# Kernel tuning notes

Hardware: AMD Instinct MI355X
Metric: run time of the kernel (lower is better)

Reference implementation:

```python
import jax, jax.numpy as jnp
import numpy as np

HEADS = 8
D_MODEL = 512
T_LEN = 12
WINDOW = 3
N_NODES = 325
BATCH = 4
HDIM = D_MODEL // HEADS
LN_EPS = 1e-5


def _shift_list(T, W):
    # matches get_shift_list: circular left shifts by W, W-1, ..., 1
    idxs = np.arange(T)
    return np.stack([(idxs + i) % T for i in range(-W, 0)])  # [W, T]


def setup_inputs() -> dict:
    key = jax.random.key(0)
    ks = jax.random.split(key, 13)
    s = 1.0 / np.sqrt(D_MODEL)
    return {
        "x": jax.random.normal(ks[0], (BATCH, T_LEN, N_NODES, D_MODEL), jnp.float32),
        "adj": jax.random.uniform(ks[1], (BATCH, T_LEN, N_NODES, N_NODES), jnp.float32),
        "s_adj": jax.random.normal(ks[2], (BATCH, N_NODES, N_NODES), jnp.float32),
        "Wq": jax.random.normal(ks[3], (D_MODEL, D_MODEL), jnp.float32) * s,
        "bq": jax.random.normal(ks[4], (D_MODEL,), jnp.float32) * 0.01,
        "Wk": jax.random.normal(ks[5], (D_MODEL, D_MODEL), jnp.float32) * s,
        "bk": jax.random.normal(ks[6], (D_MODEL,), jnp.float32) * 0.01,
        "Wv": jax.random.normal(ks[7], (D_MODEL, D_MODEL), jnp.float32) * s,
        "bv": jax.random.normal(ks[8], (D_MODEL,), jnp.float32) * 0.01,
        "Wd": jax.random.normal(ks[9], (T_LEN, T_LEN * WINDOW), jnp.float32) * (1.0 / np.sqrt(T_LEN * WINDOW)),
        "bd": jax.random.normal(ks[10], (T_LEN,), jnp.float32) * 0.01,
        "gamma": jnp.ones((D_MODEL,), jnp.float32),
        "beta": jnp.zeros((D_MODEL,), jnp.float32),
    }


def reference(x, adj, s_adj, Wq, bq, Wk, bk, Wv, bv, Wd, bd, gamma, beta):
    B, T, N, D = x.shape
    H, hd = HEADS, D // HEADS
    shifts = _shift_list(T, WINDOW)  # static numpy indices

    def proj(W_, b_):
        y = jnp.einsum("btnd,ed->btne", x, W_) + b_  # Linear: x @ W.T + b
        return y.reshape(B, T, N, H, hd).transpose(0, 1, 3, 2, 4)  # [B,T,H,N,hd]

    q = proj(Wq, bq)
    k = proj(Wk, bk)
    v = proj(Wv, bv)

    # Faithful to the original: q scaling and k/v shifts ACCUMULATE across
    # window iterations (q,k,v are reassigned in the torch loop); adj is
    # re-indexed from the original tensor each iteration.
    scale = 1.0 / jnp.asarray(np.sqrt(hd), x.dtype)
    hs = []
    qc, kc, vc = q, k, v
    for ti in range(WINDOW):
        qc = qc * scale
        s_idx = shifts[ti]
        kc = kc[:, s_idx]
        vc = vc[:, s_idx]
        a = jnp.einsum("bthnd,bthmd->bthnm", qc, kc)  # [B,T,H,N,N]
        a = (a + 1.0) * adj[:, s_idx][:, :, None, :, :]  # broadcast over heads
        a = jax.nn.softmax(a, axis=-1)
        r = jnp.einsum("bthnm,bthmd->bthnd", a, vc)
        hs.append(r.transpose(0, 1, 3, 2, 4).reshape(B, T, N, D))

    h = jnp.concatenate(hs, axis=1)          # [B, W*T, N, D]
    h = h.transpose(0, 2, 3, 1)              # [B, N, D, W*T]
    h = jnp.einsum("bndw,tw->bndt", h, Wd) + bd  # dense over time axis
    h = h.transpose(0, 3, 1, 2)              # [B, T, N, D]
    # dropout is identity at inference
    y = h + x
    mu = jnp.mean(y, axis=-1, keepdims=True)
    var = jnp.mean((y - mu) ** 2, axis=-1, keepdims=True)
    return (y - mu) / jnp.sqrt(var + LN_EPS) * gamma + beta
```

## Files before the change

### kernel.cpp

```cpp
#include <hip/hip_runtime.h>
#include <stdint.h>

#define HEADS 8
#define DM 512
#define TT 12
#define WIN 3
#define NN 325
#define BB 4
#define HD 64
#define MROWS (BB*TT*NN)
#define NSLAB (BB*TT*HEADS)
#define NKT 11
static const size_t QKV_ELE = (size_t)MROWS * DM;
static const size_t FRAG_SLAB = (size_t)NKT * 4 * 64 * 8;

typedef unsigned short u16;
typedef __attribute__((ext_vector_type(8))) short bf16x8;
typedef __attribute__((ext_vector_type(4))) float f32x4;

#define MFMA(a,b,c) __builtin_amdgcn_mfma_f32_16x16x32_bf16(a, b, c, 0, 0, 0)
#define LG2E 1.44269504f
#define C8F  (-11.5415603f)

static __device__ __forceinline__ float ex2(float x) {
  float r; asm("v_exp_f32 %0, %1" : "=v"(r) : "v"(x)); return r;
}

static __device__ __forceinline__ u16 f2bf(float f) {
  uint32_t u = __float_as_uint(f);
  u += 0x7fff + ((u >> 16) & 1);
  return (u16)(u >> 16);
}
static __device__ __forceinline__ uint32_t pk2(float hi, float lo) {
  return __builtin_amdgcn_perm(__float_as_uint(hi), __float_as_uint(lo), 0x07060302);
}
static __device__ __forceinline__ float bf2f(u16 h) {
  return __uint_as_float((uint32_t)h << 16);
}

typedef const __attribute__((address_space(1))) unsigned int* gas1;
typedef __attribute__((address_space(3))) unsigned int* las3;
static __device__ __forceinline__ void gll16(const void* g, void* l) {
  __builtin_amdgcn_global_load_lds((gas1)g, (las3)l, 16, 0, 0);
}

__global__ void pack_w(const float* __restrict__ Wq, const float* __restrict__ Wk,
                       const float* __restrict__ Wv, const float* __restrict__ bq,
                       const float* __restrict__ bk, const float* __restrict__ bv,
                       u16* __restrict__ Wb, float* __restrict__ biasc) {
  int i = blockIdx.x * blockDim.x + threadIdx.x;
  const int n4 = (3 * 512 * 512) / 4;
  if (i < n4) {
    int j = i << 2;
    int which = j >> 18;
    int off4 = i & ((512 * 512 / 4) - 1);
    const float* src = which == 0 ? Wq : (which == 1 ? Wk : Wv);
    float4 v = ((const float4*)src)[off4];
    uint32_t a0 = (uint32_t)f2bf(v.x) | ((uint32_t)f2bf(v.y) << 16);
    uint32_t a1 = (uint32_t)f2bf(v.z) | ((uint32_t)f2bf(v.w) << 16);
    ((uint2*)Wb)[i] = make_uint2(a0, a1);
  }
  if (i < 1536 / 4) {
    int j = i << 2;
    int which = j >> 9;
    int off4 = i & 127;
    const float* src = which == 0 ? bq : (which == 1 ? bk : bv);
    ((float4*)biasc)[i] = ((const float4*)src)[off4];
  }
}

__global__ __launch_bounds__(256) void proj_gemm(
    const float* __restrict__ x,
    const u16* __restrict__ W,
    const float* __restrict__ bias,
    u16* __restrict__ qkv)
{
  __shared__ u16 sA[128 * 32];
  __shared__ u16 sB[128 * 32];
  const int m0 = blockIdx.x * 128;
  const int n0 = blockIdx.y * 128;
  const int tid = threadIdx.x;
  const int lane = tid & 63;
  const int wid = tid >> 6;
  const int wr = wid >> 1, wc = wid & 1;

  f32x4 acc[4][4] = {};

  const int srow = tid >> 2;
  const int scol = (tid & 3) * 8;

  for (int k0 = 0; k0 < 512; k0 += 32) {
    __syncthreads();
#pragma unroll
    for (int i = 0; i < 2; ++i) {
      int row = i * 64 + srow;
      int gm = m0 + row; if (gm >= MROWS) gm = MROWS - 1;
      const float* xa = x + (size_t)gm * 512 + k0 + scol;
      float4 f0 = *(const float4*)xa;
      float4 f1 = *(const float4*)(xa + 4);
      uint4 u;
      u.x = pk2(f0.y, f0.x);
      u.y = pk2(f0.w, f0.z);
      u.z = pk2(f1.y, f1.x);
      u.w = pk2(f1.w, f1.z);
      *(uint4*)&sA[row * 32 + scol] = u;
      *(bf16x8*)&sB[row * 32 + scol] = *(const bf16x8*)&W[(size_t)(n0 + row) * 512 + k0 + scol];
    }
    __syncthreads();
    bf16x8 af[4], bfr[4];
#pragma unroll
    for (int mi = 0; mi < 4; ++mi)
      af[mi] = *(const bf16x8*)&sA[(wr * 64 + mi * 16 + (lane & 15)) * 32 + (lane >> 4) * 8];
#pragma unroll
    for (int ni = 0; ni < 4; ++ni)
      bfr[ni] = *(const bf16x8*)&sB[(wc * 64 + ni * 16 + (lane & 15)) * 32 + (lane >> 4) * 8];
#pragma unroll
    for (int mi = 0; mi < 4; ++mi)
#pragma unroll
      for (int ni = 0; ni < 4; ++ni)
        acc[mi][ni] = MFMA(af[mi], bfr[ni], acc[mi][ni]);
  }

  const int lr = (lane >> 4) * 4;
  const int lc = lane & 15;
#pragma unroll
  for (int mi = 0; mi < 4; ++mi) {
#pragma unroll
    for (int j = 0; j < 4; ++j) {
      int gm = m0 + wr * 64 + mi * 16 + lr + j;
      if (gm < MROWS) {
        int b = gm / (TT * NN);
        int rem = gm - b * (TT * NN);
        int t = rem / NN;
        int n = rem - t * NN;
#pragma unroll
        for (int ni = 0; ni < 4; ++ni) {
          int e = n0 + wc * 64 + ni * 16 + lc;
          float val = acc[mi][ni][j] + bias[e];
          int which = e >> 9;
          int h = (e >> 6) & 7;
          int d = e & 63;
          qkv[(size_t)which * QKV_ELE + ((((size_t)(b * TT + t) * HEADS + h) * NN + n) << 6) + d] = f2bf(val);
        }
      }
    }
  }
}

__global__ __launch_bounds__(256) void kv_pack(const u16* __restrict__ qkv,
                                               u16* __restrict__ kf, u16* __restrict__ vf) {
  int slab = blockIdx.x;
  const u16* K = qkv + QKV_ELE + ((size_t)slab * NN << 6);
  const u16* V = qkv + 2 * QKV_ELE + ((size_t)slab * NN << 6);
  u16* kout = kf + (size_t)slab * FRAG_SLAB;
  u16* vout = vf + (size_t)slab * FRAG_SLAB;
  int t = threadIdx.x;
  int f = t >> 6;
  int lane = t & 63;
  int qi = lane & 15, g = lane >> 4;
  int krow_l = ((qi >> 2) << 3) + (qi & 3) + ((f >> 1) << 2);
  int kd = ((f & 1) << 5) + g * 8;
  for (int kt = 0; kt < NKT; ++kt) {
    int row = kt * 32 + krow_l;
    bf16x8 kv = {};
    if (row < NN) kv = *(const bf16x8*)(K + ((size_t)row << 6) + kd);
    *(bf16x8*)(kout + ((size_t)kt * 4 + f) * 512 + lane * 8) = kv;
    union { u16 e[8]; bf16x8 v; } vv;
#pragma unroll
    for (int e = 0; e < 8; ++e) {
      int vrow = kt * 32 + g * 8 + e;
      vv.e[e] = (vrow < NN) ? V[((size_t)vrow << 6) + f * 16 + qi] : (u16)0;
    }
    *(bf16x8*)(vout + ((size_t)kt * 4 + f) * 512 + lane * 8) = vv.v;
  }
}

__global__ __launch_bounds__(256) void adj_pack(const float* __restrict__ adj,
                                                float* __restrict__ adjp) {
  int blk = blockIdx.x;
  int kt = blk % 11;
  int rest = blk / 11;
  int qt = rest % 6;
  int slab = rest / 6;
  const float* src = adj + (size_t)slab * NN * NN;
  float* dst = adjp + (size_t)blk * 2048;
  int t = threadIdx.x;
  int s = t >> 6, lane = t & 63;
  int qi = lane & 15, g = lane >> 4;
  int row = qt * 64 + s * 16 + qi; if (row > NN - 1) row = NN - 1;
  int c0 = kt * 32 + g * 8;
  const float* sp = src + (size_t)row * NN;
  float v[8];
#pragma unroll
  for (int e = 0; e < 8; ++e) {
    int c = c0 + e;
    v[e] = (c < NN) ? __builtin_fmaf(sp[c], LG2E, C8F) : C8F;
  }
  float4 w0 = {v[0], v[1], v[2], v[3]};
  float4 w1 = {v[4], v[5], v[6], v[7]};
  *(float4*)(dst + t * 8) = w0;
  *(float4*)(dst + t * 8 + 4) = w1;
}

__global__ __launch_bounds__(256, 2) void attn(
    const u16* __restrict__ q,
    const u16* __restrict__ kf,
    const u16* __restrict__ vf,
    const float* __restrict__ adjp,
    u16* __restrict__ hcat)
{
  __shared__ u16 kvlds[4][2][2][4][512];

  const int tid = threadIdx.x;
  const int wid = tid >> 6;
  const int lane = tid & 63;
  const int qi = lane & 15;
  const int g = lane >> 4;

  int ord = (blockIdx.x & 7) * 216 + (blockIdx.x >> 3);
  int slab = ord / 36;
  int inner = ord - slab * 36;
  int b = slab / 12;
  int ta = slab - b * 12;
  int ti = inner / 12;
  int r2 = inner - ti * 12;
  int qt = r2 >> 1;
  int hg = r2 & 1;

  int tadd = ti == 0 ? 3 : (ti == 1 ? 2 : 1);
  int ckv  = ti == 0 ? 9 : (ti == 1 ? 7 : 6);
  float qsc = ti == 0 ? 0.125f : (ti == 1 ? 0.015625f : 0.001953125f);
  int t = ta + tadd; if (t >= 12) t -= 12;
  int t_kv = t + ckv; if (t_kv >= 12) t_kv -= 12;
  int h = hg * 4 + wid;
  int q0 = qt * 64;

  const float nqC8 = -qsc * C8F;

  const u16* qbase = q + ((((size_t)(b * TT + t) * HEADS + h) * NN) << 6);
  int kvslab = (b * TT + t_kv) * HEADS + h;
  const u16* kfb = kf + (size_t)kvslab * FRAG_SLAB + lane * 8;
  const u16* vfb = vf + (size_t)kvslab * FRAG_SLAB + lane * 8;
  const float* apb = adjp + (size_t)(slab * 6 + qt) * (11 * 2048) + lane * 8;

  bf16x8 qf[4][2];
#pragma unroll
  for (int s = 0; s < 4; ++s) {
    int qr = q0 + s * 16 + qi; if (qr > NN - 1) qr = NN - 1;
    const u16* qp = qbase + ((size_t)qr << 6) + g * 8;
    qf[s][0] = *(const bf16x8*)qp;
    qf[s][1] = *(const bf16x8*)(qp + 32);
  }

  const f32x4 z4 = {0.f, 0.f, 0.f, 0.f};

  f32x4 acc[4][4] = {};
  float lsum[4] = {0.f, 0.f, 0.f, 0.f};

#pragma unroll
  for (int f = 0; f < 4; ++f) {
    gll16(kfb + (size_t)f * 512, &kvlds[wid][0][0][f][0]);
    gll16(vfb + (size_t)f * 512, &kvlds[wid][0][1][f][0]);
  }
  float4 fa[4], fb4[4];
#pragma unroll
  for (int s = 0; s < 4; ++s) {
    fa[s]  = *(const float4*)(apb + s * 512);
    fb4[s] = *(const float4*)(apb + s * 512 + 4);
  }

  for (int kt = 0; kt < 11; ++kt) {
    int cur = kt & 1;
    float4 fan[4], fbn[4];
    if (kt < 10) {
      const u16* kp = kfb + (size_t)(kt + 1) * 2048;
      const u16* vp = vfb + (size_t)(kt + 1) * 2048;
#pragma unroll
      for (int f = 0; f < 4; ++f) {
        gll16(kp + (size_t)f * 512, &kvlds[wid][cur ^ 1][0][f][0]);
        gll16(vp + (size_t)f * 512, &kvlds[wid][cur ^ 1][1][f][0]);
      }
      const float* ap = apb + (size_t)(kt + 1) * 2048;
#pragma unroll
      for (int s = 0; s < 4; ++s) {
        fan[s] = *(const float4*)(ap + s * 512);
        fbn[s] = *(const float4*)(ap + s * 512 + 4);
      }
      asm volatile("s_waitcnt vmcnt(16)" ::: "memory");
    } else {
      asm volatile("s_waitcnt vmcnt(0)" ::: "memory");
    }

    bf16x8 kc[4], vc[4];
#pragma unroll
    for (int f = 0; f < 4; ++f) {
      kc[f] = *(const bf16x8*)&kvlds[wid][cur][0][f][lane * 8];
      vc[f] = *(const bf16x8*)&kvlds[wid][cur][1][f][lane * 8];
    }

#pragma unroll
    for (int s = 0; s < 4; ++s) {
      f32x4 s0 = MFMA(kc[0], qf[s][0], z4);
      s0 = MFMA(kc[1], qf[s][1], s0);
      f32x4 s1 = MFMA(kc[2], qf[s][0], z4);
      s1 = MFMA(kc[3], qf[s][1], s1);
      float p[8];
      float u, qu;
      u = fa[s].x;  qu = __builtin_fmaf(qsc, u, nqC8); p[0] = ex2(__builtin_fmaf(s0[0], qu, u));
      u = fa[s].y;  qu = __builtin_fmaf(qsc, u, nqC8); p[1] = ex2(__builtin_fmaf(s0[1], qu, u));
      u = fa[s].z;  qu = __builtin_fmaf(qsc, u, nqC8); p[2] = ex2(__builtin_fmaf(s0[2], qu, u));
      u = fa[s].w;  qu = __builtin_fmaf(qsc, u, nqC8); p[3] = ex2(__builtin_fmaf(s0[3], qu, u));
      u = fb4[s].x; qu = __builtin_fmaf(qsc, u, nqC8); p[4] = ex2(__builtin_fmaf(s1[0], qu, u));
      u = fb4[s].y; qu = __builtin_fmaf(qsc, u, nqC8); p[5] = ex2(__builtin_fmaf(s1[1], qu, u));
      u = fb4[s].z; qu = __builtin_fmaf(qsc, u, nqC8); p[6] = ex2(__builtin_fmaf(s1[2], qu, u));
      u = fb4[s].w; qu = __builtin_fmaf(qsc, u, nqC8); p[7] = ex2(__builtin_fmaf(s1[3], qu, u));
      lsum[s] += ((p[0] + p[1]) + (p[2] + p[3])) + ((p[4] + p[5]) + (p[6] + p[7]));
      union { uint32_t u[4]; bf16x8 v; } pu;
      pu.u[0] = pk2(p[1], p[0]);
      pu.u[1] = pk2(p[3], p[2]);
      pu.u[2] = pk2(p[5], p[4]);
      pu.u[3] = pk2(p[7], p[6]);
      acc[s][0] = MFMA(pu.v, vc[0], acc[s][0]);
      acc[s][1] = MFMA(pu.v, vc[1], acc[s][1]);
      acc[s][2] = MFMA(pu.v, vc[2], acc[s][2]);
      acc[s][3] = MFMA(pu.v, vc[3], acc[s][3]);
    }
#pragma unroll
    for (int s = 0; s < 4; ++s) { fa[s] = fan[s]; fb4[s] = fbn[s]; }
  }

  const float padcorr = 27.0f * ex2(C8F);
  size_t hb = ((size_t)(b * 36 + ti * TT + t) * NN) << 9;
#pragma unroll
  for (int s = 0; s < 4; ++s) {
    float v = lsum[s];
    v += __shfl_xor(v, 16);
    v += __shfl_xor(v, 32);
    v -= padcorr;
    float linv = 1.0f / v;
#pragma unroll
    for (int j = 0; j < 4; ++j) {
      float li = __shfl(linv, g * 4 + j);
      int qrow = q0 + s * 16 + 4 * g + j;
      if (qrow < NN) {
        u16* op = hcat + hb + ((size_t)qrow << 9) + h * 64 + qi;
#pragma unroll
        for (int dt = 0; dt < 4; ++dt)
          op[dt * 16] = f2bf(acc[s][dt][j] * li);
      }
    }
  }
}

__global__ __launch_bounds__(256, 4) void mix_ln(
    const u16* __restrict__ hcat,
    const float* __restrict__ Wd,
    const float* __restrict__ bd,
    const float* __restrict__ x,
    const float* __restrict__ gamma,
    const float* __restrict__ beta,
    float* __restrict__ out)
{
  __shared__ u16 sH[36 * 512];
  __shared__ float sWd[12 * 36];
  __shared__ float sred[8];
  int bn = blockIdx.x;
  int b = bn / NN, n = bn - b * NN;
  int tid = threadIdx.x;
  int lane = tid & 63, wid = tid >> 6;

  for (int i = tid; i < 12 * 36; i += 256) sWd[i] = Wd[i];
  for (int i = tid; i < 36 * 128; i += 256) {
    int w = i >> 7, d4 = i & 127;
    *(uint2*)&sH[(w << 9) + (d4 << 2)] =
        *(const uint2*)&hcat[(((size_t)(b * 36 + w) * NN + n) << 9) + (d4 << 2)];
  }
  __syncthreads();

  for (int t = 0; t < TT; ++t) {
    float a0 = 0.f, a1 = 0.f;
#pragma unroll
    for (int w = 0; w < 36; ++w) {
      float wv = sWd[t * 36 + w];
      a0 += bf2f(sH[(w << 9) + tid]) * wv;
      a1 += bf2f(sH[(w << 9) + 256 + tid]) * wv;
    }
    size_t xoff = ((size_t)(b * TT + t) * NN + n) << 9;
    float bdt = bd[t];
    float y0 = a0 + bdt + x[xoff + tid];
    float y1 = a1 + bdt + x[xoff + 256 + tid];
    float s = y0 + y1, ss = y0 * y0 + y1 * y1;
#pragma unroll
    for (int off = 32; off > 0; off >>= 1) {
      s += __shfl_down(s, off);
      ss += __shfl_down(ss, off);
    }
    if (lane == 0) { sred[wid * 2] = s; sred[wid * 2 + 1] = ss; }
    __syncthreads();
    float stot = sred[0] + sred[2] + sred[4] + sred[6];
    float sstot = sred[1] + sred[3] + sred[5] + sred[7];
    float mu = stot * (1.0f / 512.0f);
    float var = sstot * (1.0f / 512.0f) - mu * mu;
    float rstd = rsqrtf(var + 1e-5f);
    out[xoff + tid] = (y0 - mu) * rstd * gamma[tid] + beta[tid];
    out[xoff + 256 + tid] = (y1 - mu) * rstd * gamma[tid + 256] + beta[tid + 256];
    __syncthreads();
  }
}

extern "C" void kernel_launch(void* const* d_in, const int* in_sizes, int n_in,
                              void* d_out, int out_size, void* d_ws, size_t ws_size,
                              hipStream_t stream) {
  const float* x     = (const float*)d_in[0];
  const float* adj   = (const float*)d_in[1];
  const float* Wq    = (const float*)d_in[3];
  const float* bq    = (const float*)d_in[4];
  const float* Wk    = (const float*)d_in[5];
  const float* bk    = (const float*)d_in[6];
  const float* Wv    = (const float*)d_in[7];
  const float* bv    = (const float*)d_in[8];
  const float* Wd    = (const float*)d_in[9];
  const float* bd    = (const float*)d_in[10];
  const float* gamma = (const float*)d_in[11];
  const float* beta  = (const float*)d_in[12];
  float* out = (float*)d_out;

  char* ws = (char*)d_ws;
  size_t off = 0;
  auto alloc = [&](size_t bytes) {
    void* p = ws + off;
    off += (bytes + 255) & ~(size_t)255;
    return p;
  };
  u16* Wb     = (u16*)alloc(1536 * 512 * 2);
  float* bias = (float*)alloc(1536 * 4);
  u16* qkv    = (u16*)alloc(3 * QKV_ELE * 2);
  u16* hcat   = (u16*)alloc(3 * QKV_ELE * 2);
  u16* kfb    = (u16*)alloc((size_t)NSLAB * FRAG_SLAB * 2);
  u16* vfb    = (u16*)alloc((size_t)NSLAB * FRAG_SLAB * 2);
  float* adjp = (float*)alloc((size_t)48 * 6 * 11 * 2048 * 4);

  adj_pack<<<dim3(48 * 6 * 11), dim3(256), 0, stream>>>(adj, adjp);
  pack_w<<<dim3(768), dim3(256), 0, stream>>>(Wq, Wk, Wv, bq, bk, bv, Wb, bias);
  proj_gemm<<<dim3((MROWS + 127) / 128, 1536 / 128), dim3(256), 0, stream>>>(x, Wb, bias, qkv);
  kv_pack<<<dim3(NSLAB), dim3(256), 0, stream>>>(qkv, kfb, vfb);
  attn<<<dim3(BB * TT * WIN * 6 * 2), dim3(256), 0, stream>>>(qkv, kfb, vfb, adjp, hcat);
  mix_ln<<<dim3(BB * NN), dim3(256), 0, stream>>>(hcat, Wd, bd, x, gamma, beta, out);
}
```

Measured before the change: 223.4 us.

## Merge prep kernels, swizzle projection GEMM blocks, make layer-norm wave-per-timestep

Folds the adjacency packing and weight packing into one launch to save a kernel launch. The projection GEMM now uses a 1D grid with an XCD-aware swizzle of block order, which should improve L2 reuse of the weight and activation tiles. mix_ln is restructured so each wave handles whole timesteps with 8 contiguous features per lane: it uses vectorized bf16x8 LDS reads and float4 global loads and stores, and the reduction becomes a wave-level xor shuffle. This removes the per-timestep block barriers and shared-memory reductions. The cost is more registers per thread in mix_ln.

```diff
diff --git a/kernel.cpp b/kernel.cpp
--- a/kernel.cpp
+++ b/kernel.cpp
@@ -44,28 +44,56 @@
   __builtin_amdgcn_global_load_lds((gas1)g, (las3)l, 16, 0, 0);
 }
 
-__global__ void pack_w(const float* __restrict__ Wq, const float* __restrict__ Wk,
-                       const float* __restrict__ Wv, const float* __restrict__ bq,
-                       const float* __restrict__ bk, const float* __restrict__ bv,
-                       u16* __restrict__ Wb, float* __restrict__ biasc) {
-  int i = blockIdx.x * blockDim.x + threadIdx.x;
-  const int n4 = (3 * 512 * 512) / 4;
-  if (i < n4) {
-    int j = i << 2;
-    int which = j >> 18;
-    int off4 = i & ((512 * 512 / 4) - 1);
-    const float* src = which == 0 ? Wq : (which == 1 ? Wk : Wv);
-    float4 v = ((const float4*)src)[off4];
-    uint32_t a0 = (uint32_t)f2bf(v.x) | ((uint32_t)f2bf(v.y) << 16);
-    uint32_t a1 = (uint32_t)f2bf(v.z) | ((uint32_t)f2bf(v.w) << 16);
-    ((uint2*)Wb)[i] = make_uint2(a0, a1);
-  }
-  if (i < 1536 / 4) {
-    int j = i << 2;
-    int which = j >> 9;
-    int off4 = i & 127;
-    const float* src = which == 0 ? bq : (which == 1 ? bk : bv);
-    ((float4*)biasc)[i] = ((const float4*)src)[off4];
+__global__ __launch_bounds__(256) void prep(
+    const float* __restrict__ adj, const float* __restrict__ Wq,
+    const float* __restrict__ Wk, const float* __restrict__ Wv,
+    const float* __restrict__ bq, const float* __restrict__ bk,
+    const float* __restrict__ bv, float* __restrict__ adjp,
+    u16* __restrict__ Wb, float* __restrict__ biasc) {
+  if (blockIdx.x < 3168) {
+    int blk = blockIdx.x;
+    int kt = blk % 11;
+    int rest = blk / 11;
+    int qt = rest % 6;
+    int slab = rest / 6;
+    const float* src = adj + (size_t)slab * NN * NN;
+    float* dst = adjp + (size_t)blk * 2048;
+    int t = threadIdx.x;
+    int s = t >> 6, lane = t & 63;
+    int qi = lane & 15, g = lane >> 4;
+    int row = qt * 64 + s * 16 + qi; if (row > NN - 1) row = NN - 1;
+    int c0 = kt * 32 + g * 8;
+    const float* sp = src + (size_t)row * NN;
+    float v[8];
+#pragma unroll
+    for (int e = 0; e < 8; ++e) {
+      int c = c0 + e;
+      v[e] = (c < NN) ? __builtin_fmaf(sp[c], LG2E, C8F) : C8F;
+    }
+    float4 w0 = {v[0], v[1], v[2], v[3]};
+    float4 w1 = {v[4], v[5], v[6], v[7]};
+    *(float4*)(dst + t * 8) = w0;
+    *(float4*)(dst + t * 8 + 4) = w1;
+  } else {
+    int i = (blockIdx.x - 3168) * 256 + threadIdx.x;
+    const int n4 = (3 * 512 * 512) / 4;
+    if (i < n4) {
+      int j = i << 2;
+      int which = j >> 18;
+      int off4 = i & ((512 * 512 / 4) - 1);
+      const float* src = which == 0 ? Wq : (which == 1 ? Wk : Wv);
+      float4 v = ((const float4*)src)[off4];
+      uint32_t a0 = (uint32_t)f2bf(v.x) | ((uint32_t)f2bf(v.y) << 16);
+      uint32_t a1 = (uint32_t)f2bf(v.z) | ((uint32_t)f2bf(v.w) << 16);
+      ((uint2*)Wb)[i] = make_uint2(a0, a1);
+    }
+    if (i < 1536 / 4) {
+      int j = i << 2;
+      int which = j >> 9;
+      int off4 = i & 127;
+      const float* src = which == 0 ? bq : (which == 1 ? bk : bv);
+      ((float4*)biasc)[i] = ((const float4*)src)[off4];
+    }
   }
 }
 
@@ -77,8 +105,10 @@
 {
   __shared__ u16 sA[128 * 32];
   __shared__ u16 sB[128 * 32];
-  const int m0 = blockIdx.x * 128;
-  const int n0 = blockIdx.y * 128;
+  int bid = blockIdx.x;
+  int ord = (bid & 7) * 183 + (bid >> 3);
+  const int m0 = (ord / 12) * 128;
+  const int n0 = (ord % 12) * 128;
   const int tid = threadIdx.x;
   const int lane = tid & 63;
   const int wid = tid >> 6;
@@ -173,33 +203,6 @@
     }
     *(bf16x8*)(vout + ((size_t)kt * 4 + f) * 512 + lane * 8) = vv.v;
   }
-}
-
-__global__ __launch_bounds__(256) void adj_pack(const float* __restrict__ adj,
-                                                float* __restrict__ adjp) {
-  int blk = blockIdx.x;
-  int kt = blk % 11;
-  int rest = blk / 11;
-  int qt = rest % 6;
-  int slab = rest / 6;
-  const float* src = adj + (size_t)slab * NN * NN;
-  float* dst = adjp + (size_t)blk * 2048;
-  int t = threadIdx.x;
-  int s = t >> 6, lane = t & 63;
-  int qi = lane & 15, g = lane >> 4;
-  int row = qt * 64 + s * 16 + qi; if (row > NN - 1) row = NN - 1;
-  int c0 = kt * 32 + g * 8;
-  const float* sp = src + (size_t)row * NN;
-  float v[8];
-#pragma unroll
-  for (int e = 0; e < 8; ++e) {
-    int c = c0 + e;
-    v[e] = (c < NN) ? __builtin_fmaf(sp[c], LG2E, C8F) : C8F;
-  }
-  float4 w0 = {v[0], v[1], v[2], v[3]};
-  float4 w1 = {v[4], v[5], v[6], v[7]};
-  *(float4*)(dst + t * 8) = w0;
-  *(float4*)(dst + t * 8 + 4) = w1;
 }
 
 __global__ __launch_bounds__(256, 2) void attn(
@@ -363,7 +366,6 @@
 {
   __shared__ u16 sH[36 * 512];
   __shared__ float sWd[12 * 36];
-  __shared__ float sred[8];
   int bn = blockIdx.x;
   int b = bn / NN, n = bn - b * NN;
   int tid = threadIdx.x;
@@ -377,34 +379,53 @@
   }
   __syncthreads();
 
-  for (int t = 0; t < TT; ++t) {
-    float a0 = 0.f, a1 = 0.f;
-#pragma unroll
+  const int d0 = lane * 8;
+  float4 g0 = *(const float4*)&gamma[d0];
+  float4 g1 = *(const float4*)&gamma[d0 + 4];
+  float4 be0 = *(const float4*)&beta[d0];
+  float4 be1 = *(const float4*)&beta[d0 + 4];
+
+  for (int t = wid; t < TT; t += 4) {
+    float a[8] = {};
+    const float* wrow = &sWd[t * 36];
+#pragma unroll 4
     for (int w = 0; w < 36; ++w) {
-      float wv = sWd[t * 36 + w];
-      a0 += bf2f(sH[(w << 9) + tid]) * wv;
-      a1 += bf2f(sH[(w << 9) + 256 + tid]) * wv;
+      float wv = wrow[w];
+      bf16x8 hv = *(const bf16x8*)&sH[(w << 9) + d0];
+#pragma unroll
+      for (int j = 0; j < 8; ++j) a[j] = __builtin_fmaf(bf2f((u16)hv[j]), wv, a[j]);
     }
     size_t xoff = ((size_t)(b * TT + t) * NN + n) << 9;
+    float4 x0 = *(const float4*)&x[xoff + d0];
+    float4 x1 = *(const float4*)&x[xoff + d0 + 4];
     float bdt = bd[t];
-    float y0 = a0 + bdt + x[xoff + tid];
-    float y1 = a1 + bdt + x[xoff + 256 + tid];
-    float s = y0 + y1, ss = y0 * y0 + y1 * y1;
+    float y[8];
+    y[0] = a[0] + bdt + x0.x;  y[1] = a[1] + bdt + x0.y;
+    y[2] = a[2] + bdt + x0.z;  y[3] = a[3] + bdt + x0.w;
+    y[4] = a[4] + bdt + x1.x;  y[5] = a[5] + bdt + x1.y;
+    y[6] = a[6] + bdt + x1.z;  y[7] = a[7] + bdt + x1.w;
+    float s = 0.f, ss = 0.f;
+#pragma unroll
+    for (int j = 0; j < 8; ++j) { s += y[j]; ss = __builtin_fmaf(y[j], y[j], ss); }
 #pragma unroll
     for (int off = 32; off > 0; off >>= 1) {
-      s += __shfl_down(s, off);
-      ss += __shfl_down(ss, off);
-    }
-    if (lane == 0) { sred[wid * 2] = s; sred[wid * 2 + 1] = ss; }
-    __syncthreads();
-    float stot = sred[0] + sred[2] + sred[4] + sred[6];
-    float sstot = sred[1] + sred[3] + sred[5] + sred[7];
-    float mu = stot * (1.0f / 512.0f);
-    float var = sstot * (1.0f / 512.0f) - mu * mu;
+      s += __shfl_xor(s, off);
+      ss += __shfl_xor(ss, off);
+    }
+    float mu = s * (1.0f / 512.0f);
+    float var = ss * (1.0f / 512.0f) - mu * mu;
     float rstd = rsqrtf(var + 1e-5f);
-    out[xoff + tid] = (y0 - mu) * rstd * gamma[tid] + beta[tid];
-    out[xoff + 256 + tid] = (y1 - mu) * rstd * gamma[tid + 256] + beta[tid + 256];
-    __syncthreads();
+    float4 o0, o1;
+    o0.x = (y[0] - mu) * rstd * g0.x + be0.x;
+    o0.y = (y[1] - mu) * rstd * g0.y + be0.y;
+    o0.z = (y[2] - mu) * rstd * g0.z + be0.z;
+    o0.w = (y[3] - mu) * rstd * g0.w + be0.w;
+    o1.x = (y[4] - mu) * rstd * g1.x + be1.x;
+    o1.y = (y[5] - mu) * rstd * g1.y + be1.y;
+    o1.z = (y[6] - mu) * rstd * g1.z + be1.z;
+    o1.w = (y[7] - mu) * rstd * g1.w + be1.w;
+    *(float4*)&out[xoff + d0] = o0;
+    *(float4*)&out[xoff + d0 + 4] = o1;
   }
 }
 
@@ -440,9 +461,8 @@
   u16* vfb    = (u16*)alloc((size_t)NSLAB * FRAG_SLAB * 2);
   float* adjp = (float*)alloc((size_t)48 * 6 * 11 * 2048 * 4);
 
-  adj_pack<<<dim3(48 * 6 * 11), dim3(256), 0, stream>>>(adj, adjp);
-  pack_w<<<dim3(768), dim3(256), 0, stream>>>(Wq, Wk, Wv, bq, bk, bv, Wb, bias);
-  proj_gemm<<<dim3((MROWS + 127) / 128, 1536 / 128), dim3(256), 0, stream>>>(x, Wb, bias, qkv);
+  prep<<<dim3(3168 + 768), dim3(256), 0, stream>>>(adj, Wq, Wk, Wv, bq, bk, bv, adjp, Wb, bias);
+  proj_gemm<<<dim3(1464), dim3(256), 0, stream>>>(x, Wb, bias, qkv);
   kv_pack<<<dim3(NSLAB), dim3(256), 0, stream>>>(qkv, kfb, vfb);
   attn<<<dim3(BB * TT * WIN * 6 * 2), dim3(256), 0, stream>>>(qkv, kfb, vfb, adjp, hcat);
   mix_ln<<<dim3(BB * NN), dim3(256), 0, stream>>>(hcat, Wd, bd, x, gamma, beta, out);
```

After: 188.9 us. -15.5%, faster.
